# Optimization experiments

Measured on AMD Instinct MI355X. Metric: run time of the kernel, lower is better.

Reference implementation:

```python
import jax, jax.numpy as jnp
import numpy as np

VOC_SIZE = 50000
WORD_DIM = 64
CPR_DIM = 64
NUM_RELS = 7
BATCH = 1024
N_LEAVES = 64  # complete binary tree, depth 6
BOUND = 0.05


def setup_inputs() -> dict:
    key = jax.random.key(0)
    ks = jax.random.split(key, 16)
    u = lambda k, shape: jax.random.uniform(k, shape, jnp.float32, -BOUND, BOUND)
    return {
        "left_leaves": jax.random.randint(ks[0], (BATCH, N_LEAVES), 0, VOC_SIZE),
        "right_leaves": jax.random.randint(ks[1], (BATCH, N_LEAVES), 0, VOC_SIZE),
        "voc_w": u(ks[2], (WORD_DIM, VOC_SIZE)),
        "voc_b": u(ks[3], (WORD_DIM,)),
        "cps_w": u(ks[4], (WORD_DIM, 2 * WORD_DIM)),
        "cps_b": u(ks[5], (WORD_DIM,)),
        "cpst_w": u(ks[6], (WORD_DIM, WORD_DIM * WORD_DIM)),
        "cpst_b": u(ks[7], (WORD_DIM,)),
        "cpr_w": u(ks[8], (CPR_DIM, 2 * WORD_DIM)),
        "cpr_b": u(ks[9], (CPR_DIM,)),
        "cprt_w": u(ks[10], (CPR_DIM, WORD_DIM * WORD_DIM)),
        "cprt_b": u(ks[11], (CPR_DIM,)),
        "sm_w": u(ks[12], (NUM_RELS, CPR_DIM)),
        "sm_b": u(ks[13], (NUM_RELS,)),
    }


def _compose(x, cps_w, cps_b, cpst_w, cpst_b):
    # x: [B, N, d] leaf embeddings of a complete binary tree; reduce level by level.
    B, N, d = x.shape
    while N > 1:
        L = x[:, 0::2, :]  # [B, N/2, d]
        R = x[:, 1::2, :]
        cps = jnp.einsum("bnf,ef->bne", jnp.concatenate([L, R], axis=-1), cps_w) + cps_b
        # NOTE: source computes ger(left, left) for interior nodes (left with itself)
        kron = (L[:, :, :, None] * L[:, :, None, :]).reshape(B, N // 2, d * d)
        cps_t = jnp.einsum("bnk,ek->bne", kron, cpst_w) + cpst_b
        x = jnp.tanh(cps + cps_t)
        N //= 2
    return x[:, 0, :]  # [B, d]


def reference(left_leaves, right_leaves, voc_w, voc_b, cps_w, cps_b, cpst_w, cpst_b,
              cpr_w, cpr_b, cprt_w, cprt_b, sm_w, sm_b):
    # onehot @ Linear == embedding gather of columns of voc_w, plus bias
    left_emb = voc_w.T[left_leaves] + voc_b    # [B, N, d]
    right_emb = voc_w.T[right_leaves] + voc_b
    l = _compose(left_emb, cps_w, cps_b, cpst_w, cpst_b)   # [B, d]
    r = _compose(right_emb, cps_w, cps_b, cpst_w, cpst_b)  # [B, d]
    cpr = jnp.concatenate([l, r], axis=-1) @ cpr_w.T + cpr_b
    kron = (l[:, :, None] * r[:, None, :]).reshape(l.shape[0], -1)  # [B, d*d]
    cpr_t = kron @ cprt_w.T + cprt_b
    act = jax.nn.leaky_relu(cpr + cpr_t, negative_slope=0.01)
    logits = act @ sm_w.T + sm_b
    return jax.nn.softmax(logits, axis=-1)  # [B, num_rels]
```

## Files before the change

### kernel.cpp

```cpp
#include <hip/hip_runtime.h>
#include <hip/hip_bf16.h>
#include <cstdint>
#include <cstddef>

typedef _Float16 f16x8 __attribute__((ext_vector_type(8)));
typedef float    f32x4 __attribute__((ext_vector_type(4)));

#define VOC    50000
#define W2T    2432
#define NSTG_T 19
#define W2F    4224
#define NSTG_F 33
#define STG    8192
#define XSTR   72
#define TPW    8
#define IPW    16

__device__ __attribute__((aligned(256))) unsigned short g_vocT[(size_t)VOC * 64];
__device__ __attribute__((aligned(256))) unsigned short g_roots[2048 * 64];
__device__ __attribute__((aligned(256))) unsigned short g_cpstU[(size_t)NSTG_T * STG];
__device__ __attribute__((aligned(256))) unsigned short g_cprtU[(size_t)NSTG_F * STG];
__device__ float g_smw[7 * 64];
__device__ float g_smb[7];
__device__ float g_biasC[64];
__device__ float g_biasF[64];

#define KE(BI0,BJ0,R0,BI1,BJ1,R1) \
    ((BI0) | ((BJ0) << 3) | ((R0) << 6) | ((BI1) << 7) | ((BJ1) << 10) | ((R1) << 13))
__device__ __constant__ int g_ktab[18] = {
    KE(0,0,1, 0,1,1), KE(0,2,0, 0,3,0), KE(0,4,0, 0,5,0), KE(0,6,0, 0,7,0),
    KE(1,1,1, 1,2,1), KE(1,3,0, 1,4,0), KE(1,5,0, 1,6,0), KE(1,7,0, 2,2,1),
    KE(2,3,1, 2,4,0), KE(2,5,0, 2,6,0), KE(2,7,0, 3,3,1), KE(3,4,1, 3,5,0),
    KE(3,6,0, 3,7,0), KE(4,4,1, 4,5,1), KE(4,6,0, 4,7,0), KE(5,5,1, 5,6,1),
    KE(5,7,0, 6,6,1), KE(6,7,1, 7,7,1)
};

__device__ __forceinline__ float b2f(unsigned short u) {
    unsigned int x = ((unsigned int)u) << 16;
    return __builtin_bit_cast(float, x);
}
__device__ __forceinline__ unsigned short f2b(float f) {
    return __builtin_bit_cast(unsigned short, (__bf16)f);
}
__device__ __forceinline__ unsigned short f2h(float f) {
    return __builtin_bit_cast(unsigned short, (_Float16)f);
}
__device__ __forceinline__ float scrub(float v) {
    return fminf(fmaxf(v, -64.f), 64.f);
}
__device__ __forceinline__ float ldf(const void* p, size_t i, int isb) {
    return isb ? b2f(((const unsigned short*)p)[i]) : ((const float*)p)[i];
}
__device__ __forceinline__ int detect_isb(const void* voc_b) {
    const unsigned int* p = (const unsigned int*)voc_b;
    int ok = 1;
    for (int k = 0; k < 32; k++) {
        float v = b2f((unsigned short)(p[k] & 0xFFFFu));
        if (!(fabsf(v) <= 0.0502f)) ok = 0;
    }
    return ok;
}

__global__ __launch_bounds__(256) void k_prep(
    const void* voc_w, const void* voc_b,
    const void* cps_w, const void* cps_b, const void* cpst_w, const void* cpst_b,
    const void* cpr_w, const void* cpr_b, const void* cprt_w, const void* cprt_b,
    const void* sm_w, const void* sm_b)
{
    __shared__ float tile[64][65];
    __shared__ float vb[64];
    const int isb = detect_isb(voc_b);
    if (blockIdx.x < 512) {
        int gid = blockIdx.x * 256 + threadIdx.x;
        int stride = 512 * 256;
        for (int d = gid; d < 64 * W2T; d += stride) {
            int s    = d / STG;
            int rem  = d - s * STG;
            int kbl  = rem >> 11;
            int rem2 = rem & 2047;
            int nt   = rem2 >> 9;
            int rem3 = rem2 & 511;
            int q    = rem3 >> 7;
            int rem4 = rem3 & 127;
            int sub  = rem4 >> 3;
            int z    = rem4 & 7;
            int n    = nt * 16 + sub;
            int k    = s * 128 + kbl * 32 + q * 8 + z;
            float w;
            if (k < 2304) {
                int b   = k >> 6;
                int p2l = (k >> 5) & 1;
                int bi = 0, remb = b;
                while (remb >= 8 - bi) { remb -= 8 - bi; bi++; }
                int bj = bi + remb;
                int i = bi * 8 + z;
                int j = bj * 8 + 2 * q + p2l;
                w = ldf(cpst_w, (size_t)n * 4096 + i * 64 + j, isb);
                if (bi != bj)
                    w += ldf(cpst_w, (size_t)n * 4096 + j * 64 + i, isb);
            } else {
                w = ldf(cps_w, (size_t)n * 128 + (k - 2304), isb);
            }
            g_cpstU[d] = f2h(w);
        }
        for (int d = gid; d < 64 * W2F; d += stride) {
            int s    = d / STG;
            int rem  = d - s * STG;
            int kbl  = rem >> 11;
            int rem2 = rem & 2047;
            int nt   = rem2 >> 9;
            int rem3 = rem2 & 511;
            int q    = rem3 >> 7;
            int rem4 = rem3 & 127;
            int sub  = rem4 >> 3;
            int z    = rem4 & 7;
            int n    = nt * 16 + sub;
            int k    = s * 128 + kbl * 32 + q * 8 + z;
            float v2 = (k < 4096) ? ldf(cprt_w, (size_t)n * 4096 + k, isb)
                                  : ldf(cpr_w,  (size_t)n * 128 + (k - 4096), isb);
            g_cprtU[d] = f2h(v2);
        }
        for (int i = gid; i < 448; i += stride) g_smw[i] = ldf(sm_w, i, isb);
        if (gid < 64) {
            g_biasC[gid] = ldf(cps_b, gid, isb) + ldf(cpst_b, gid, isb);
            g_biasF[gid] = ldf(cpr_b, gid, isb) + ldf(cprt_b, gid, isb);
        }
        if (gid < 7) g_smb[gid] = ldf(sm_b, gid, isb);
    } else {
        int t = threadIdx.x;
        if (t < 64) vb[t] = ldf(voc_b, t, isb);
        int v0 = (blockIdx.x - 512) * 64;
        int vl = t & 63, dr = t >> 6;
        #pragma unroll
        for (int i = 0; i < 16; i++) {
            int d = dr * 16 + i;
            int v = v0 + vl;
            tile[vl][d] = (v < VOC) ? ldf(voc_w, (size_t)d * VOC + v, isb) : 0.f;
        }
        __syncthreads();
        int dl = t & 63, vr0 = t >> 6;
        #pragma unroll
        for (int i = 0; i < 16; i++) {
            int vr = vr0 * 16 + i;
            int v = v0 + vr;
            if (v < VOC) g_vocT[(size_t)v * 64 + dl] = f2h(tile[vr][dl] + vb[dl]);
        }
    }
}

#define EPILOGUE(CO)                                                          \
    if (lv < 5) {                                                             \
        _Pragma("unroll")                                                     \
        for (int nt = 0; nt < 4; nt++) {                                      \
            int e = nt * 16 + sub;                                            \
            _Pragma("unroll")                                                 \
            for (int rr = 0; rr < 4; rr++) {                                  \
                int m = chv[CO] * 16 + q * 4 + rr;                            \
                if (m < nodes) {                                              \
                    int t2 = m >> lg, n2 = m & (cnew - 1);                    \
                    Xs[(t2 * 64 + n2) * XSTR + e] =                           \
                        f2h(tanhf(scrub(acc[CO][nt][rr] + biasC[e])));        \
                }                                                             \
            }                                                                 \
        }                                                                     \
    } else {                                                                  \
        _Pragma("unroll")                                                     \
        for (int nt = 0; nt < 4; nt++) {                                      \
            int e = nt * 16 + sub;                                            \
            _Pragma("unroll")                                                 \
            for (int rr = 0; rr < 4; rr++) {                                  \
                int m = q * 4 + rr;                                           \
                if (m < TPW)                                                  \
                    g_roots[((size_t)wg * TPW + m) * 64 + e] =                \
                        f2h(tanhf(scrub(acc[CO][nt][rr] + biasC[e])));        \
            }                                                                 \
        }                                                                     \
    }

#define EXSEND(CS)                                                            \
    { _Pragma("unroll")                                                       \
      for (int nt = 0; nt < 4; nt++)                                          \
          *(f32x4*)(exchS + wave * 1024 + nt * 256 + lane * 4) = acc[CS][nt]; }

#define EXRECV(CO)                                                            \
    { _Pragma("unroll")                                                       \
      for (int nt = 0; nt < 4; nt++) {                                        \
          f32x4 v_ = *(const f32x4*)(exchS + (wave ^ 1) * 1024 + nt * 256 + lane * 4); \
          _Pragma("unroll")                                                   \
          for (int z = 0; z < 4; z++) acc[CO][nt][z] += v_[z];                \
      } }

#define BLD8(BF, SBASE)                                                       \
    { const unsigned short* gs_ = (SBASE) + half * 4096 + lane * 8;           \
      _Pragma("unroll")                                                       \
      for (int j = 0; j < 8; j++)                                             \
          BF[j] = *(const f16x8*)(gs_ + (j >> 2) * 2048 + (j & 3) * 512); }

#define KMM(CI, AV, B0, B1, B2, B3)                                           \
    { f16x8 a_ = (AV);                                                        \
      acc[CI][0] = __builtin_amdgcn_mfma_f32_16x16x32_f16(a_, B0, acc[CI][0], 0, 0, 0); \
      acc[CI][1] = __builtin_amdgcn_mfma_f32_16x16x32_f16(a_, B1, acc[CI][1], 0, 0, 0); \
      acc[CI][2] = __builtin_amdgcn_mfma_f32_16x16x32_f16(a_, B2, acc[CI][2], 0, 0, 0); \
      acc[CI][3] = __builtin_amdgcn_mfma_f32_16x16x32_f16(a_, B3, acc[CI][3], 0, 0, 0); }

#define KBLOCKR(BF, BI, BJ, RLD)                                              \
    if (act[0]) {                                                             \
        if (RLD) {                                                            \
            lA0 = *(const f16x8*)(Xs + slotL[0] + (BI) * 8);                  \
            if (act[1]) lA1 = *(const f16x8*)(Xs + slotL[1] + (BI) * 8);      \
            if (act[2]) lA2 = *(const f16x8*)(Xs + slotL[2] + (BI) * 8);      \
            if (act[3]) lA3 = *(const f16x8*)(Xs + slotL[3] + (BI) * 8);      \
        }                                                                     \
        _Float16 sc0[4], sc1[4];                                              \
        _Pragma("unroll")                                                     \
        for (int c = 0; c < 4; c++)                                           \
            if (act[c]) {                                                     \
                unsigned pr_ = *(const unsigned*)(Xs + slotL[c] + (BJ) * 8 + 2 * q); \
                sc0[c] = __builtin_bit_cast(_Float16, (unsigned short)(pr_ & 0xFFFFu)); \
                sc1[c] = __builtin_bit_cast(_Float16, (unsigned short)(pr_ >> 16));     \
            }                                                                 \
        _Pragma("unroll")                                                     \
        for (int p2 = 0; p2 < 2; p2++) {                                      \
            KMM(0, lA0 * (p2 ? sc1[0] : sc0[0]),                              \
                BF[p2 * 4 + 0], BF[p2 * 4 + 1], BF[p2 * 4 + 2], BF[p2 * 4 + 3]) \
            if (act[1]) KMM(1, lA1 * (p2 ? sc1[1] : sc0[1]),                  \
                BF[p2 * 4 + 0], BF[p2 * 4 + 1], BF[p2 * 4 + 2], BF[p2 * 4 + 3]) \
            if (act[2]) KMM(2, lA2 * (p2 ? sc1[2] : sc0[2]),                  \
                BF[p2 * 4 + 0], BF[p2 * 4 + 1], BF[p2 * 4 + 2], BF[p2 * 4 + 3]) \
            if (act[3]) KMM(3, lA3 * (p2 ? sc1[3] : sc0[3]),                  \
                BF[p2 * 4 + 0], BF[p2 * 4 + 1], BF[p2 * 4 + 2], BF[p2 * 4 + 3]) \
        }                                                                     \
    }

#define KRUNR(S, BF)                                                          \
    {                                                                         \
        int e_   = g_ktab[S];                                                 \
        int ent_ = half ? (e_ >> 7) : e_;                                     \
        int bi_  = ent_ & 7;                                                  \
        int bj_  = (ent_ >> 3) & 7;                                           \
        int rld_ = (ent_ >> 6) & 1;                                           \
        KBLOCKR((BF), bi_, bj_, rld_)                                         \
    }

__global__ __launch_bounds__(512, 2)
void k_tree(const int* __restrict__ lleaf, const int* __restrict__ rleaf)
{
    __shared__ __attribute__((aligned(16))) unsigned short Xs[512 * XSTR];
    __shared__ __attribute__((aligned(16))) float exchS[8192];
    __shared__ float biasC[64];
    const int tid = threadIdx.x;
    const int wg  = blockIdx.x;

    if (tid < 64) biasC[tid] = g_biasC[tid];

    {
        int t = tid >> 6, i = tid & 63;
        int gidx = wg * TPW + t;
        int b = (gidx < 1024) ? gidx : gidx - 1024;
        const int* lv2 = (gidx < 1024) ? lleaf : rleaf;
        int idx = lv2[b * 64 + i];
        idx = (idx < 0) ? 0 : ((idx >= VOC) ? VOC - 1 : idx);
        const uint4* src = (const uint4*)(g_vocT + (size_t)idx * 64);
        uint4* dst = (uint4*)(Xs + tid * XSTR);
        #pragma unroll
        for (int z = 0; z < 8; z++) dst[z] = src[z];
    }

    __syncthreads();

    const int lane = tid & 63, wave = tid >> 6;
    const int q = lane >> 4, sub = lane & 15;
    const int p = wave >> 1, half = wave & 1;

    #pragma unroll 1
    for (int lv = 0; lv < 6; lv++) {
        const int lg = 5 - lv;
        const int cnew = 1 << lg;
        const int nodes = TPW << lg;
        const int nchunks = (nodes + 15) >> 4;

        int act[4], chv[4], slotL[4];
        #pragma unroll
        for (int c = 0; c < 4; c++) {
            int ch = p + 4 * c;
            act[c] = (ch < nchunks);
            chv[c] = ch;
            int m = ch * 16 + sub;
            if (!act[c] || m >= nodes) m = 0;
            int t = m >> lg, n = m & (cnew - 1);
            slotL[c] = (t * 64 + 2 * n) * XSTR;
        }

        f16x8 lA0 = {}, lA1 = {}, lA2 = {}, lA3 = {};
        f32x4 acc[4][4];
        #pragma unroll
        for (int c = 0; c < 4; c++)
            #pragma unroll
            for (int nt = 0; nt < 4; nt++)
                #pragma unroll
                for (int z = 0; z < 4; z++) acc[c][nt][z] = 0.f;

        f16x8 bfA[8], bfB[8];
        if (act[0]) BLD8(bfA, g_cpstU)
        #pragma unroll 1
        for (int t = 0; t < 9; t++) {
            if (act[0]) BLD8(bfB, g_cpstU + (size_t)(2 * t + 1) * STG)
            KRUNR(2 * t, bfA)
            if (act[0]) BLD8(bfA, g_cpstU + (size_t)(2 * t + 2) * STG)
            KRUNR(2 * t + 1, bfB)
        }

        if (act[0]) {
            #pragma unroll
            for (int p2 = 0; p2 < 2; p2++) {
                #pragma unroll
                for (int c = 0; c < 4; c++) {
                    if (!act[c]) continue;
                    f16x8 A = *(const f16x8*)(Xs + slotL[c] + half * XSTR + p2 * 32 + q * 8);
                    acc[c][0] = __builtin_amdgcn_mfma_f32_16x16x32_f16(A, bfA[p2 * 4 + 0], acc[c][0], 0, 0, 0);
                    acc[c][1] = __builtin_amdgcn_mfma_f32_16x16x32_f16(A, bfA[p2 * 4 + 1], acc[c][1], 0, 0, 0);
                    acc[c][2] = __builtin_amdgcn_mfma_f32_16x16x32_f16(A, bfA[p2 * 4 + 2], acc[c][2], 0, 0, 0);
                    acc[c][3] = __builtin_amdgcn_mfma_f32_16x16x32_f16(A, bfA[p2 * 4 + 3], acc[c][3], 0, 0, 0);
                }
            }
        }

        if (half == 0) { if (act[1]) EXSEND(1) } else { if (act[0]) EXSEND(0) }
        __syncthreads();
        if (half == 0) {
            if (act[0]) { EXRECV(0) EPILOGUE(0) }
        } else {
            if (act[1]) { EXRECV(1) EPILOGUE(1) }
        }
        __syncthreads();
        if (half == 0) { if (act[3]) EXSEND(3) } else { if (act[2]) EXSEND(2) }
        __syncthreads();
        if (half == 0) {
            if (act[2]) { EXRECV(2) EPILOGUE(2) }
        } else {
            if (act[3]) { EXRECV(3) EPILOGUE(3) }
        }
        __syncthreads();
    }
}

#define BLD4(BF, S)                                                           \
    { const unsigned short* gs_ = g_cprtU + (size_t)(S) * STG + w * 512 + lane * 8; \
      _Pragma("unroll")                                                       \
      for (int j = 0; j < 4; j++)                                             \
          BF[j] = *(const f16x8*)(gs_ + j * 2048); }

#define FKRONR(S, BF)                                                         \
    { _Pragma("unroll")                                                       \
      for (int ii = 0; ii < 2; ii++) {                                        \
          int i_ = 2 * (S) + ii;                                              \
          _Float16 li_ = __builtin_bit_cast(_Float16, Lv[rowLo + i_]);        \
          _Pragma("unroll")                                                   \
          for (int p2 = 0; p2 < 2; p2++) {                                    \
              f16x8 afr_ = Ra[p2] * li_;                                      \
              acc = __builtin_amdgcn_mfma_f32_16x16x32_f16(afr_, BF[2 * ii + p2], acc, 0, 0, 0); \
          }                                                                   \
      } }

__global__ __launch_bounds__(256, 2) void k_final(const void* __restrict__ voc_b,
                                                  void* __restrict__ out)
{
    __shared__ __attribute__((aligned(16))) unsigned short Lv[IPW * XSTR], Rv[IPW * XSTR];
    __shared__ float actS[IPW][65];
    __shared__ float smw[7][64];
    __shared__ float smbS[7];
    __shared__ float biasF[64];
    const int tid = threadIdx.x, wg = blockIdx.x;
    const int isb = detect_isb(voc_b);

    if (tid < 64) biasF[tid] = g_biasF[tid];
    if (tid < 7)  smbS[tid] = g_smb[tid];
    for (int z = tid; z < 448; z += 256) smw[z >> 6][z & 63] = g_smw[z];

    {
        int side = tid >> 7, idx = tid & 127;
        int item = idx >> 3, piece = idx & 7;
        const uint4* s4 = (const uint4*)(g_roots +
            ((size_t)(side * 1024) + (size_t)wg * IPW + item) * 64 + piece * 8);
        uint4* d4 = (uint4*)((side ? Rv : Lv) + item * XSTR + piece * 8);
        *d4 = *s4;
    }

    const int lane = tid & 63, w = tid >> 6;
    const int q = lane >> 4, sub = lane & 15;
    const int rowLo = sub * XSTR;

    f16x8 bA[4], bB[4];
    BLD4(bA, 0)

    __syncthreads();

    f16x8 Ra[2];
    Ra[0] = *(const f16x8*)(Rv + rowLo + q * 8);
    Ra[1] = *(const f16x8*)(Rv + rowLo + 32 + q * 8);

    f32x4 acc;
    #pragma unroll
    for (int z = 0; z < 4; z++) acc[z] = 0.f;

    #pragma unroll 1
    for (int t = 0; t < 16; t++) {
        BLD4(bB, 2 * t + 1)
        FKRONR(2 * t, bA)
        BLD4(bA, 2 * t + 2)
        FKRONR(2 * t + 1, bB)
    }

    {
        f16x8 A4[4];
        A4[0] = *(const f16x8*)(Lv + rowLo + q * 8);
        A4[1] = *(const f16x8*)(Lv + rowLo + 32 + q * 8);
        A4[2] = *(const f16x8*)(Rv + rowLo + q * 8);
        A4[3] = *(const f16x8*)(Rv + rowLo + 32 + q * 8);
        #pragma unroll
        for (int kbl = 0; kbl < 4; kbl++)
            acc = __builtin_amdgcn_mfma_f32_16x16x32_f16(A4[kbl], bA[kbl], acc, 0, 0, 0);
    }

    {
        int e = w * 16 + sub;
        #pragma unroll
        for (int rr = 0; rr < 4; rr++) {
            int item = q * 4 + rr;
            float v = scrub(acc[rr] + biasF[e]);
            v = (v > 0.f) ? v : 0.01f * v;
            actS[item][e] = v;
        }
    }
    __syncthreads();

    if (tid < IPW) {
        float lg[7];
        #pragma unroll
        for (int j = 0; j < 7; j++) lg[j] = smbS[j];
        for (int e = 0; e < 64; e++) {
            float a = actS[tid][e];
            #pragma unroll
            for (int j = 0; j < 7; j++) lg[j] += smw[j][e] * a;
        }
        float mx = lg[0];
        #pragma unroll
        for (int j = 1; j < 7; j++) mx = fmaxf(mx, lg[j]);
        float s = 0.f, pr[7];
        #pragma unroll
        for (int j = 0; j < 7; j++) { pr[j] = expf(lg[j] - mx); s += pr[j]; }
        float inv = 1.f / s;
        size_t b = (size_t)wg * IPW + tid;
        if (isb) {
            unsigned short* o = (unsigned short*)out;
            #pragma unroll
            for (int j = 0; j < 7; j++) o[b * 7 + j] = f2b(pr[j] * inv);
        } else {
            float* o = (float*)out;
            #pragma unroll
            for (int j = 0; j < 7; j++) o[b * 7 + j] = pr[j] * inv;
        }
    }
}

extern "C" void kernel_launch(void* const* d_in, const int* in_sizes, int n_in,
                              void* d_out, int out_size, void* d_ws, size_t ws_size,
                              hipStream_t stream) {
    const int* lleaf = (const int*)d_in[0];
    const int* rleaf = (const int*)d_in[1];
    const void* voc_w  = d_in[2];
    const void* voc_b  = d_in[3];
    const void* cps_w  = d_in[4];
    const void* cps_b  = d_in[5];
    const void* cpst_w = d_in[6];
    const void* cpst_b = d_in[7];
    const void* cpr_w  = d_in[8];
    const void* cpr_b  = d_in[9];
    const void* cprt_w = d_in[10];
    const void* cprt_b = d_in[11];
    const void* sm_w   = d_in[12];
    const void* sm_b   = d_in[13];

    k_prep<<<512 + (VOC + 63) / 64, 256, 0, stream>>>(
        voc_w, voc_b, cps_w, cps_b, cpst_w, cpst_b,
        cpr_w, cpr_b, cprt_w, cprt_b, sm_w, sm_b);
    k_tree<<<2048 / TPW, 512, 0, stream>>>(lleaf, rleaf);
    k_final<<<64, 256, 0, stream>>>(voc_b, (unsigned short*)d_out);
}
```

Baseline: 177.3 us.

## Fuse prep, tree and final kernels into one cooperative persistent kernel

Merges the three launches (weight/vocab prep, tree composition, final classifier) into one cooperative kernel of 256 blocks of 512 threads, using grid-wide syncs between phases. Shared memory is reused across phases, for example the transpose tile is aliased onto Xs. This removes the launch gaps between kernels and the tail idle time of each one. In exchange, the vocabulary transpose now runs on fewer blocks, occupancy is limited by cooperative-launch residency rules, and each grid sync has its own cost.

```diff
diff --git a/kernel.cpp b/kernel.cpp
--- a/kernel.cpp
+++ b/kernel.cpp
@@ -1,7 +1,10 @@
 #include <hip/hip_runtime.h>
 #include <hip/hip_bf16.h>
+#include <hip/hip_cooperative_groups.h>
 #include <cstdint>
 #include <cstddef>
+
+namespace cg = cooperative_groups;
 
 typedef _Float16 f16x8 __attribute__((ext_vector_type(8)));
 typedef float    f32x4 __attribute__((ext_vector_type(4)));
@@ -61,18 +64,136 @@
     return ok;
 }
 
-__global__ __launch_bounds__(256) void k_prep(
-    const void* voc_w, const void* voc_b,
-    const void* cps_w, const void* cps_b, const void* cpst_w, const void* cpst_b,
-    const void* cpr_w, const void* cpr_b, const void* cprt_w, const void* cprt_b,
-    const void* sm_w, const void* sm_b)
+#define EPILOGUE(CO)                                                          \
+    if (lv < 5) {                                                             \
+        _Pragma("unroll")                                                     \
+        for (int nt = 0; nt < 4; nt++) {                                      \
+            int e = nt * 16 + sub;                                            \
+            _Pragma("unroll")                                                 \
+            for (int rr = 0; rr < 4; rr++) {                                  \
+                int m = chv[CO] * 16 + q * 4 + rr;                            \
+                if (m < nodes) {                                              \
+                    int t2 = m >> lg, n2 = m & (cnew - 1);                    \
+                    Xs[(t2 * 64 + n2) * XSTR + e] =                           \
+                        f2h(tanhf(scrub(acc[CO][nt][rr] + biasC[e])));        \
+                }                                                             \
+            }                                                                 \
+        }                                                                     \
+    } else {                                                                  \
+        _Pragma("unroll")                                                     \
+        for (int nt = 0; nt < 4; nt++) {                                      \
+            int e = nt * 16 + sub;                                            \
+            _Pragma("unroll")                                                 \
+            for (int rr = 0; rr < 4; rr++) {                                  \
+                int m = q * 4 + rr;                                           \
+                if (m < TPW)                                                  \
+                    g_roots[((size_t)wg * TPW + m) * 64 + e] =                \
+                        f2h(tanhf(scrub(acc[CO][nt][rr] + biasC[e])));        \
+            }                                                                 \
+        }                                                                     \
+    }
+
+#define EXSEND(CS)                                                            \
+    { _Pragma("unroll")                                                       \
+      for (int nt = 0; nt < 4; nt++)                                          \
+          *(f32x4*)(exchS + wave * 1024 + nt * 256 + lane * 4) = acc[CS][nt]; }
+
+#define EXRECV(CO)                                                            \
+    { _Pragma("unroll")                                                       \
+      for (int nt = 0; nt < 4; nt++) {                                        \
+          f32x4 v_ = *(const f32x4*)(exchS + (wave ^ 1) * 1024 + nt * 256 + lane * 4); \
+          _Pragma("unroll")                                                   \
+          for (int z = 0; z < 4; z++) acc[CO][nt][z] += v_[z];                \
+      } }
+
+#define BLD8(BF, SBASE)                                                       \
+    { const unsigned short* gs_ = (SBASE) + half * 4096 + lane * 8;           \
+      _Pragma("unroll")                                                       \
+      for (int j = 0; j < 8; j++)                                             \
+          BF[j] = *(const f16x8*)(gs_ + (j >> 2) * 2048 + (j & 3) * 512); }
+
+#define KMM(CI, AV, B0, B1, B2, B3)                                           \
+    { f16x8 a_ = (AV);                                                        \
+      acc[CI][0] = __builtin_amdgcn_mfma_f32_16x16x32_f16(a_, B0, acc[CI][0], 0, 0, 0); \
+      acc[CI][1] = __builtin_amdgcn_mfma_f32_16x16x32_f16(a_, B1, acc[CI][1], 0, 0, 0); \
+      acc[CI][2] = __builtin_amdgcn_mfma_f32_16x16x32_f16(a_, B2, acc[CI][2], 0, 0, 0); \
+      acc[CI][3] = __builtin_amdgcn_mfma_f32_16x16x32_f16(a_, B3, acc[CI][3], 0, 0, 0); }
+
+#define KBLOCKR(BF, BI, BJ, RLD)                                              \
+    if (act[0]) {                                                             \
+        if (RLD) {                                                            \
+            lA0 = *(const f16x8*)(Xs + slotL[0] + (BI) * 8);                  \
+            if (act[1]) lA1 = *(const f16x8*)(Xs + slotL[1] + (BI) * 8);      \
+            if (act[2]) lA2 = *(const f16x8*)(Xs + slotL[2] + (BI) * 8);      \
+            if (act[3]) lA3 = *(const f16x8*)(Xs + slotL[3] + (BI) * 8);      \
+        }                                                                     \
+        _Float16 sc0[4], sc1[4];                                              \
+        _Pragma("unroll")                                                     \
+        for (int c = 0; c < 4; c++)                                           \
+            if (act[c]) {                                                     \
+                unsigned pr_ = *(const unsigned*)(Xs + slotL[c] + (BJ) * 8 + 2 * q); \
+                sc0[c] = __builtin_bit_cast(_Float16, (unsigned short)(pr_ & 0xFFFFu)); \
+                sc1[c] = __builtin_bit_cast(_Float16, (unsigned short)(pr_ >> 16));     \
+            }                                                                 \
+        _Pragma("unroll")                                                     \
+        for (int p2 = 0; p2 < 2; p2++) {                                      \
+            KMM(0, lA0 * (p2 ? sc1[0] : sc0[0]),                              \
+                BF[p2 * 4 + 0], BF[p2 * 4 + 1], BF[p2 * 4 + 2], BF[p2 * 4 + 3]) \
+            if (act[1]) KMM(1, lA1 * (p2 ? sc1[1] : sc0[1]),                  \
+                BF[p2 * 4 + 0], BF[p2 * 4 + 1], BF[p2 * 4 + 2], BF[p2 * 4 + 3]) \
+            if (act[2]) KMM(2, lA2 * (p2 ? sc1[2] : sc0[2]),                  \
+                BF[p2 * 4 + 0], BF[p2 * 4 + 1], BF[p2 * 4 + 2], BF[p2 * 4 + 3]) \
+            if (act[3]) KMM(3, lA3 * (p2 ? sc1[3] : sc0[3]),                  \
+                BF[p2 * 4 + 0], BF[p2 * 4 + 1], BF[p2 * 4 + 2], BF[p2 * 4 + 3]) \
+        }                                                                     \
+    }
+
+#define KRUNR(S, BF)                                                          \
+    {                                                                         \
+        int e_   = g_ktab[S];                                                 \
+        int ent_ = half ? (e_ >> 7) : e_;                                     \
+        int bi_  = ent_ & 7;                                                  \
+        int bj_  = (ent_ >> 3) & 7;                                           \
+        int rld_ = (ent_ >> 6) & 1;                                           \
+        KBLOCKR((BF), bi_, bj_, rld_)                                         \
+    }
+
+#define BLD4(BF, S)                                                           \
+    { const unsigned short* gs_ = g_cprtU + (size_t)(S) * STG + w * 512 + lane * 8; \
+      _Pragma("unroll")                                                       \
+      for (int j = 0; j < 4; j++)                                             \
+          BF[j] = *(const f16x8*)(gs_ + j * 2048); }
+
+#define FKRONR(S, BF)                                                         \
+    { _Pragma("unroll")                                                       \
+      for (int ii = 0; ii < 2; ii++) {                                        \
+          int i_ = 2 * (S) + ii;                                              \
+          _Float16 li_ = __builtin_bit_cast(_Float16, Lv[rowLo + i_]);        \
+          _Pragma("unroll")                                                   \
+          for (int p2 = 0; p2 < 2; p2++) {                                    \
+              f16x8 afr_ = Ra[p2] * li_;                                      \
+              accF = __builtin_amdgcn_mfma_f32_16x16x32_f16(afr_, BF[2 * ii + p2], accF, 0, 0, 0); \
+          }                                                                   \
+      } }
+
+__global__ __launch_bounds__(512, 2)
+void k_all(const int* __restrict__ lleaf, const int* __restrict__ rleaf,
+           const void* __restrict__ voc_w, const void* __restrict__ voc_b,
+           const void* cps_w, const void* cps_b, const void* cpst_w, const void* cpst_b,
+           const void* cpr_w, const void* cpr_b, const void* cprt_w, const void* cprt_b,
+           const void* sm_w, const void* sm_b, void* __restrict__ out)
 {
-    __shared__ float tile[64][65];
-    __shared__ float vb[64];
+    __shared__ __attribute__((aligned(16))) unsigned short Xs[512 * XSTR];
+    __shared__ __attribute__((aligned(16))) float exchS[8192];
+    __shared__ float biasC[64];
+    const int tid = threadIdx.x;
+    const int wg  = blockIdx.x;
     const int isb = detect_isb(voc_b);
-    if (blockIdx.x < 512) {
-        int gid = blockIdx.x * 256 + threadIdx.x;
-        int stride = 512 * 256;
+    cg::grid_group grid = cg::this_grid();
+
+    {
+        int gid = wg * 512 + tid;
+        const int stride = 256 * 512;
         for (int d = gid; d < 64 * W2T; d += stride) {
             int s    = d / STG;
             int rem  = d - s * STG;
@@ -126,133 +247,35 @@
             g_biasF[gid] = ldf(cpr_b, gid, isb) + ldf(cprt_b, gid, isb);
         }
         if (gid < 7) g_smb[gid] = ldf(sm_b, gid, isb);
-    } else {
-        int t = threadIdx.x;
-        if (t < 64) vb[t] = ldf(voc_b, t, isb);
-        int v0 = (blockIdx.x - 512) * 64;
-        int vl = t & 63, dr = t >> 6;
-        #pragma unroll
-        for (int i = 0; i < 16; i++) {
-            int d = dr * 16 + i;
-            int v = v0 + vl;
-            tile[vl][d] = (v < VOC) ? ldf(voc_w, (size_t)d * VOC + v, isb) : 0.f;
-        }
+
+        float* tileF = (float*)Xs;
+        float* vbF   = exchS;
+        if (tid < 64) vbF[tid] = ldf(voc_b, tid, isb);
         __syncthreads();
-        int dl = t & 63, vr0 = t >> 6;
-        #pragma unroll
-        for (int i = 0; i < 16; i++) {
-            int vr = vr0 * 16 + i;
-            int v = v0 + vr;
-            if (v < VOC) g_vocT[(size_t)v * 64 + dl] = f2h(tile[vr][dl] + vb[dl]);
-        }
-    }
-}
-
-#define EPILOGUE(CO)                                                          \
-    if (lv < 5) {                                                             \
-        _Pragma("unroll")                                                     \
-        for (int nt = 0; nt < 4; nt++) {                                      \
-            int e = nt * 16 + sub;                                            \
-            _Pragma("unroll")                                                 \
-            for (int rr = 0; rr < 4; rr++) {                                  \
-                int m = chv[CO] * 16 + q * 4 + rr;                            \
-                if (m < nodes) {                                              \
-                    int t2 = m >> lg, n2 = m & (cnew - 1);                    \
-                    Xs[(t2 * 64 + n2) * XSTR + e] =                           \
-                        f2h(tanhf(scrub(acc[CO][nt][rr] + biasC[e])));        \
-                }                                                             \
-            }                                                                 \
-        }                                                                     \
-    } else {                                                                  \
-        _Pragma("unroll")                                                     \
-        for (int nt = 0; nt < 4; nt++) {                                      \
-            int e = nt * 16 + sub;                                            \
-            _Pragma("unroll")                                                 \
-            for (int rr = 0; rr < 4; rr++) {                                  \
-                int m = q * 4 + rr;                                           \
-                if (m < TPW)                                                  \
-                    g_roots[((size_t)wg * TPW + m) * 64 + e] =                \
-                        f2h(tanhf(scrub(acc[CO][nt][rr] + biasC[e])));        \
-            }                                                                 \
-        }                                                                     \
-    }
-
-#define EXSEND(CS)                                                            \
-    { _Pragma("unroll")                                                       \
-      for (int nt = 0; nt < 4; nt++)                                          \
-          *(f32x4*)(exchS + wave * 1024 + nt * 256 + lane * 4) = acc[CS][nt]; }
-
-#define EXRECV(CO)                                                            \
-    { _Pragma("unroll")                                                       \
-      for (int nt = 0; nt < 4; nt++) {                                        \
-          f32x4 v_ = *(const f32x4*)(exchS + (wave ^ 1) * 1024 + nt * 256 + lane * 4); \
-          _Pragma("unroll")                                                   \
-          for (int z = 0; z < 4; z++) acc[CO][nt][z] += v_[z];                \
-      } }
-
-#define BLD8(BF, SBASE)                                                       \
-    { const unsigned short* gs_ = (SBASE) + half * 4096 + lane * 8;           \
-      _Pragma("unroll")                                                       \
-      for (int j = 0; j < 8; j++)                                             \
-          BF[j] = *(const f16x8*)(gs_ + (j >> 2) * 2048 + (j & 3) * 512); }
-
-#define KMM(CI, AV, B0, B1, B2, B3)                                           \
-    { f16x8 a_ = (AV);                                                        \
-      acc[CI][0] = __builtin_amdgcn_mfma_f32_16x16x32_f16(a_, B0, acc[CI][0], 0, 0, 0); \
-      acc[CI][1] = __builtin_amdgcn_mfma_f32_16x16x32_f16(a_, B1, acc[CI][1], 0, 0, 0); \
-      acc[CI][2] = __builtin_amdgcn_mfma_f32_16x16x32_f16(a_, B2, acc[CI][2], 0, 0, 0); \
-      acc[CI][3] = __builtin_amdgcn_mfma_f32_16x16x32_f16(a_, B3, acc[CI][3], 0, 0, 0); }
-
-#define KBLOCKR(BF, BI, BJ, RLD)                                              \
-    if (act[0]) {                                                             \
-        if (RLD) {                                                            \
-            lA0 = *(const f16x8*)(Xs + slotL[0] + (BI) * 8);                  \
-            if (act[1]) lA1 = *(const f16x8*)(Xs + slotL[1] + (BI) * 8);      \
-            if (act[2]) lA2 = *(const f16x8*)(Xs + slotL[2] + (BI) * 8);      \
-            if (act[3]) lA3 = *(const f16x8*)(Xs + slotL[3] + (BI) * 8);      \
-        }                                                                     \
-        _Float16 sc0[4], sc1[4];                                              \
-        _Pragma("unroll")                                                     \
-        for (int c = 0; c < 4; c++)                                           \
-            if (act[c]) {                                                     \
-                unsigned pr_ = *(const unsigned*)(Xs + slotL[c] + (BJ) * 8 + 2 * q); \
-                sc0[c] = __builtin_bit_cast(_Float16, (unsigned short)(pr_ & 0xFFFFu)); \
-                sc1[c] = __builtin_bit_cast(_Float16, (unsigned short)(pr_ >> 16));     \
-            }                                                                 \
-        _Pragma("unroll")                                                     \
-        for (int p2 = 0; p2 < 2; p2++) {                                      \
-            KMM(0, lA0 * (p2 ? sc1[0] : sc0[0]),                              \
-                BF[p2 * 4 + 0], BF[p2 * 4 + 1], BF[p2 * 4 + 2], BF[p2 * 4 + 3]) \
-            if (act[1]) KMM(1, lA1 * (p2 ? sc1[1] : sc0[1]),                  \
-                BF[p2 * 4 + 0], BF[p2 * 4 + 1], BF[p2 * 4 + 2], BF[p2 * 4 + 3]) \
-            if (act[2]) KMM(2, lA2 * (p2 ? sc1[2] : sc0[2]),                  \
-                BF[p2 * 4 + 0], BF[p2 * 4 + 1], BF[p2 * 4 + 2], BF[p2 * 4 + 3]) \
-            if (act[3]) KMM(3, lA3 * (p2 ? sc1[3] : sc0[3]),                  \
-                BF[p2 * 4 + 0], BF[p2 * 4 + 1], BF[p2 * 4 + 2], BF[p2 * 4 + 3]) \
-        }                                                                     \
-    }
-
-#define KRUNR(S, BF)                                                          \
-    {                                                                         \
-        int e_   = g_ktab[S];                                                 \
-        int ent_ = half ? (e_ >> 7) : e_;                                     \
-        int bi_  = ent_ & 7;                                                  \
-        int bj_  = (ent_ >> 3) & 7;                                           \
-        int rld_ = (ent_ >> 6) & 1;                                           \
-        KBLOCKR((BF), bi_, bj_, rld_)                                         \
-    }
-
-__global__ __launch_bounds__(512, 2)
-void k_tree(const int* __restrict__ lleaf, const int* __restrict__ rleaf)
-{
-    __shared__ __attribute__((aligned(16))) unsigned short Xs[512 * XSTR];
-    __shared__ __attribute__((aligned(16))) float exchS[8192];
-    __shared__ float biasC[64];
-    const int tid = threadIdx.x;
-    const int wg  = blockIdx.x;
+        for (int vt = wg; vt < (VOC + 63) / 64; vt += 256) {
+            int v0 = vt * 64;
+            int vl = tid & 63, dr = tid >> 6;
+            #pragma unroll
+            for (int i = 0; i < 8; i++) {
+                int d = dr * 8 + i;
+                int v = v0 + vl;
+                tileF[vl * 65 + d] = (v < VOC) ? ldf(voc_w, (size_t)d * VOC + v, isb) : 0.f;
+            }
+            __syncthreads();
+            int dl = tid & 63, vr0 = tid >> 6;
+            #pragma unroll
+            for (int i = 0; i < 8; i++) {
+                int vr = vr0 * 8 + i;
+                int v = v0 + vr;
+                if (v < VOC) g_vocT[(size_t)v * 64 + dl] = f2h(tileF[vr * 65 + dl] + vbF[dl]);
+            }
+            __syncthreads();
+        }
+    }
+    __threadfence();
+    grid.sync();
 
     if (tid < 64) biasC[tid] = g_biasC[tid];
-
     {
         int t = tid >> 6, i = tid & 63;
         int gidx = wg * TPW + t;
@@ -265,200 +288,173 @@
         #pragma unroll
         for (int z = 0; z < 8; z++) dst[z] = src[z];
     }
-
     __syncthreads();
 
-    const int lane = tid & 63, wave = tid >> 6;
-    const int q = lane >> 4, sub = lane & 15;
-    const int p = wave >> 1, half = wave & 1;
-
-    #pragma unroll 1
-    for (int lv = 0; lv < 6; lv++) {
-        const int lg = 5 - lv;
-        const int cnew = 1 << lg;
-        const int nodes = TPW << lg;
-        const int nchunks = (nodes + 15) >> 4;
-
-        int act[4], chv[4], slotL[4];
-        #pragma unroll
-        for (int c = 0; c < 4; c++) {
-            int ch = p + 4 * c;
-            act[c] = (ch < nchunks);
-            chv[c] = ch;
-            int m = ch * 16 + sub;
-            if (!act[c] || m >= nodes) m = 0;
-            int t = m >> lg, n = m & (cnew - 1);
-            slotL[c] = (t * 64 + 2 * n) * XSTR;
-        }
-
-        f16x8 lA0 = {}, lA1 = {}, lA2 = {}, lA3 = {};
-        f32x4 acc[4][4];
-        #pragma unroll
-        for (int c = 0; c < 4; c++)
-            #pragma unroll
-            for (int nt = 0; nt < 4; nt++)
-                #pragma unroll
-                for (int z = 0; z < 4; z++) acc[c][nt][z] = 0.f;
-
-        f16x8 bfA[8], bfB[8];
-        if (act[0]) BLD8(bfA, g_cpstU)
+    {
+        const int lane = tid & 63, wave = tid >> 6;
+        const int q = lane >> 4, sub = lane & 15;
+        const int p = wave >> 1, half = wave & 1;
+
         #pragma unroll 1
-        for (int t = 0; t < 9; t++) {
-            if (act[0]) BLD8(bfB, g_cpstU + (size_t)(2 * t + 1) * STG)
-            KRUNR(2 * t, bfA)
-            if (act[0]) BLD8(bfA, g_cpstU + (size_t)(2 * t + 2) * STG)
-            KRUNR(2 * t + 1, bfB)
-        }
-
-        if (act[0]) {
-            #pragma unroll
-            for (int p2 = 0; p2 < 2; p2++) {
-                #pragma unroll
-                for (int c = 0; c < 4; c++) {
-                    if (!act[c]) continue;
-                    f16x8 A = *(const f16x8*)(Xs + slotL[c] + half * XSTR + p2 * 32 + q * 8);
-                    acc[c][0] = __builtin_amdgcn_mfma_f32_16x16x32_f16(A, bfA[p2 * 4 + 0], acc[c][0], 0, 0, 0);
-                    acc[c][1] = __builtin_amdgcn_mfma_f32_16x16x32_f16(A, bfA[p2 * 4 + 1], acc[c][1], 0, 0, 0);
-                    acc[c][2] = __builtin_amdgcn_mfma_f32_16x16x32_f16(A, bfA[p2 * 4 + 2], acc[c][2], 0, 0, 0);
-                    acc[c][3] = __builtin_amdgcn_mfma_f32_16x16x32_f16(A, bfA[p2 * 4 + 3], acc[c][3], 0, 0, 0);
+        for (int lv = 0; lv < 6; lv++) {
+            const int lg = 5 - lv;
+            const int cnew = 1 << lg;
+            const int nodes = TPW << lg;
+            const int nchunks = (nodes + 15) >> 4;
+
+            int act[4], chv[4], slotL[4];
+            #pragma unroll
+            for (int c = 0; c < 4; c++) {
+                int ch = p + 4 * c;
+                act[c] = (ch < nchunks);
+                chv[c] = ch;
+                int m = ch * 16 + sub;
+                if (!act[c] || m >= nodes) m = 0;
+                int t = m >> lg, n = m & (cnew - 1);
+                slotL[c] = (t * 64 + 2 * n) * XSTR;
+            }
+
+            f16x8 lA0 = {}, lA1 = {}, lA2 = {}, lA3 = {};
+            f32x4 acc[4][4];
+            #pragma unroll
+            for (int c = 0; c < 4; c++)
+                #pragma unroll
+                for (int nt = 0; nt < 4; nt++)
+                    #pragma unroll
+                    for (int z = 0; z < 4; z++) acc[c][nt][z] = 0.f;
+
+            f16x8 bfA[8], bfB[8];
+            if (act[0]) BLD8(bfA, g_cpstU)
+            #pragma unroll 1
+            for (int t = 0; t < 9; t++) {
+                if (act[0]) BLD8(bfB, g_cpstU + (size_t)(2 * t + 1) * STG)
+                KRUNR(2 * t, bfA)
+                if (act[0]) BLD8(bfA, g_cpstU + (size_t)(2 * t + 2) * STG)
+                KRUNR(2 * t + 1, bfB)
+            }
+            if (act[0]) {
+                #pragma unroll
+                for (int p2 = 0; p2 < 2; p2++) {
+                    #pragma unroll
+                    for (int c = 0; c < 4; c++) {
+                        if (!act[c]) continue;
+                        f16x8 A = *(const f16x8*)(Xs + slotL[c] + half * XSTR + p2 * 32 + q * 8);
+                        acc[c][0] = __builtin_amdgcn_mfma_f32_16x16x32_f16(A, bfA[p2 * 4 + 0], acc[c][0], 0, 0, 0);
+                        acc[c][1] = __builtin_amdgcn_mfma_f32_16x16x32_f16(A, bfA[p2 * 4 + 1], acc[c][1], 0, 0, 0);
+                        acc[c][2] = __builtin_amdgcn_mfma_f32_16x16x32_f16(A, bfA[p2 * 4 + 2], acc[c][2], 0, 0, 0);
+                        acc[c][3] = __builtin_amdgcn_mfma_f32_16x16x32_f16(A, bfA[p2 * 4 + 3], acc[c][3], 0, 0, 0);
+                    }
                 }
             }
-        }
-
-        if (half == 0) { if (act[1]) EXSEND(1) } else { if (act[0]) EXSEND(0) }
+
+            if (half == 0) { if (act[1]) EXSEND(1) } else { if (act[0]) EXSEND(0) }
+            __syncthreads();
+            if (half == 0) {
+                if (act[0]) { EXRECV(0) EPILOGUE(0) }
+            } else {
+                if (act[1]) { EXRECV(1) EPILOGUE(1) }
+            }
+            __syncthreads();
+            if (half == 0) { if (act[3]) EXSEND(3) } else { if (act[2]) EXSEND(2) }
+            __syncthreads();
+            if (half == 0) {
+                if (act[2]) { EXRECV(2) EPILOGUE(2) }
+            } else {
+                if (act[3]) { EXRECV(3) EPILOGUE(3) }
+            }
+            __syncthreads();
+        }
+    }
+    __threadfence();
+    grid.sync();
+
+    if (wg < 64) {
+        unsigned short* Lv = Xs;
+        unsigned short* Rv = Xs + IPW * XSTR;
+        float* actS  = exchS;
+        float* smwS  = exchS + 1040;
+        float* smbS  = exchS + 1488;
+        float* biasF = exchS + 1496;
+
+        if (tid < 64) biasF[tid] = g_biasF[tid];
+        if (tid < 7)  smbS[tid] = g_smb[tid];
+        for (int z = tid; z < 448; z += 512) smwS[z] = g_smw[z];
+        if (tid < 256) {
+            int side = tid >> 7, idx = tid & 127;
+            int item = idx >> 3, piece = idx & 7;
+            const uint4* s4 = (const uint4*)(g_roots +
+                ((size_t)(side * 1024) + (size_t)wg * IPW + item) * 64 + piece * 8);
+            uint4* d4 = (uint4*)((side ? Rv : Lv) + item * XSTR + piece * 8);
+            *d4 = *s4;
+        }
         __syncthreads();
-        if (half == 0) {
-            if (act[0]) { EXRECV(0) EPILOGUE(0) }
-        } else {
-            if (act[1]) { EXRECV(1) EPILOGUE(1) }
+
+        if (tid < 256) {
+            const int lane = tid & 63, w = tid >> 6;
+            const int q = lane >> 4, sub = lane & 15;
+            const int rowLo = sub * XSTR;
+
+            f16x8 bA[4], bB[4];
+            BLD4(bA, 0)
+            f16x8 Ra[2];
+            Ra[0] = *(const f16x8*)(Rv + rowLo + q * 8);
+            Ra[1] = *(const f16x8*)(Rv + rowLo + 32 + q * 8);
+            f32x4 accF = {0.f, 0.f, 0.f, 0.f};
+
+            #pragma unroll 1
+            for (int t = 0; t < 16; t++) {
+                BLD4(bB, 2 * t + 1)
+                FKRONR(2 * t, bA)
+                BLD4(bA, 2 * t + 2)
+                FKRONR(2 * t + 1, bB)
+            }
+            {
+                f16x8 A4[4];
+                A4[0] = *(const f16x8*)(Lv + rowLo + q * 8);
+                A4[1] = *(const f16x8*)(Lv + rowLo + 32 + q * 8);
+                A4[2] = *(const f16x8*)(Rv + rowLo + q * 8);
+                A4[3] = *(const f16x8*)(Rv + rowLo + 32 + q * 8);
+                #pragma unroll
+                for (int kbl = 0; kbl < 4; kbl++)
+                    accF = __builtin_amdgcn_mfma_f32_16x16x32_f16(A4[kbl], bA[kbl], accF, 0, 0, 0);
+            }
+            int e = w * 16 + sub;
+            #pragma unroll
+            for (int rr = 0; rr < 4; rr++) {
+                int item = q * 4 + rr;
+                float v = scrub(accF[rr] + biasF[e]);
+                v = (v > 0.f) ? v : 0.01f * v;
+                actS[item * 65 + e] = v;
+            }
         }
         __syncthreads();
-        if (half == 0) { if (act[3]) EXSEND(3) } else { if (act[2]) EXSEND(2) }
-        __syncthreads();
-        if (half == 0) {
-            if (act[2]) { EXRECV(2) EPILOGUE(2) }
-        } else {
-            if (act[3]) { EXRECV(3) EPILOGUE(3) }
-        }
-        __syncthreads();
-    }
-}
-
-#define BLD4(BF, S)                                                           \
-    { const unsigned short* gs_ = g_cprtU + (size_t)(S) * STG + w * 512 + lane * 8; \
-      _Pragma("unroll")                                                       \
-      for (int j = 0; j < 4; j++)                                             \
-          BF[j] = *(const f16x8*)(gs_ + j * 2048); }
-
-#define FKRONR(S, BF)                                                         \
-    { _Pragma("unroll")                                                       \
-      for (int ii = 0; ii < 2; ii++) {                                        \
-          int i_ = 2 * (S) + ii;                                              \
-          _Float16 li_ = __builtin_bit_cast(_Float16, Lv[rowLo + i_]);        \
-          _Pragma("unroll")                                                   \
-          for (int p2 = 0; p2 < 2; p2++) {                                    \
-              f16x8 afr_ = Ra[p2] * li_;                                      \
-              acc = __builtin_amdgcn_mfma_f32_16x16x32_f16(afr_, BF[2 * ii + p2], acc, 0, 0, 0); \
-          }                                                                   \
-      } }
-
-__global__ __launch_bounds__(256, 2) void k_final(const void* __restrict__ voc_b,
-                                                  void* __restrict__ out)
-{
-    __shared__ __attribute__((aligned(16))) unsigned short Lv[IPW * XSTR], Rv[IPW * XSTR];
-    __shared__ float actS[IPW][65];
-    __shared__ float smw[7][64];
-    __shared__ float smbS[7];
-    __shared__ float biasF[64];
-    const int tid = threadIdx.x, wg = blockIdx.x;
-    const int isb = detect_isb(voc_b);
-
-    if (tid < 64) biasF[tid] = g_biasF[tid];
-    if (tid < 7)  smbS[tid] = g_smb[tid];
-    for (int z = tid; z < 448; z += 256) smw[z >> 6][z & 63] = g_smw[z];
-
-    {
-        int side = tid >> 7, idx = tid & 127;
-        int item = idx >> 3, piece = idx & 7;
-        const uint4* s4 = (const uint4*)(g_roots +
-            ((size_t)(side * 1024) + (size_t)wg * IPW + item) * 64 + piece * 8);
-        uint4* d4 = (uint4*)((side ? Rv : Lv) + item * XSTR + piece * 8);
-        *d4 = *s4;
-    }
-
-    const int lane = tid & 63, w = tid >> 6;
-    const int q = lane >> 4, sub = lane & 15;
-    const int rowLo = sub * XSTR;
-
-    f16x8 bA[4], bB[4];
-    BLD4(bA, 0)
-
-    __syncthreads();
-
-    f16x8 Ra[2];
-    Ra[0] = *(const f16x8*)(Rv + rowLo + q * 8);
-    Ra[1] = *(const f16x8*)(Rv + rowLo + 32 + q * 8);
-
-    f32x4 acc;
-    #pragma unroll
-    for (int z = 0; z < 4; z++) acc[z] = 0.f;
-
-    #pragma unroll 1
-    for (int t = 0; t < 16; t++) {
-        BLD4(bB, 2 * t + 1)
-        FKRONR(2 * t, bA)
-        BLD4(bA, 2 * t + 2)
-        FKRONR(2 * t + 1, bB)
-    }
-
-    {
-        f16x8 A4[4];
-        A4[0] = *(const f16x8*)(Lv + rowLo + q * 8);
-        A4[1] = *(const f16x8*)(Lv + rowLo + 32 + q * 8);
-        A4[2] = *(const f16x8*)(Rv + rowLo + q * 8);
-        A4[3] = *(const f16x8*)(Rv + rowLo + 32 + q * 8);
-        #pragma unroll
-        for (int kbl = 0; kbl < 4; kbl++)
-            acc = __builtin_amdgcn_mfma_f32_16x16x32_f16(A4[kbl], bA[kbl], acc, 0, 0, 0);
-    }
-
-    {
-        int e = w * 16 + sub;
-        #pragma unroll
-        for (int rr = 0; rr < 4; rr++) {
-            int item = q * 4 + rr;
-            float v = scrub(acc[rr] + biasF[e]);
-            v = (v > 0.f) ? v : 0.01f * v;
-            actS[item][e] = v;
-        }
-    }
-    __syncthreads();
-
-    if (tid < IPW) {
-        float lg[7];
-        #pragma unroll
-        for (int j = 0; j < 7; j++) lg[j] = smbS[j];
-        for (int e = 0; e < 64; e++) {
-            float a = actS[tid][e];
-            #pragma unroll
-            for (int j = 0; j < 7; j++) lg[j] += smw[j][e] * a;
-        }
-        float mx = lg[0];
-        #pragma unroll
-        for (int j = 1; j < 7; j++) mx = fmaxf(mx, lg[j]);
-        float s = 0.f, pr[7];
-        #pragma unroll
-        for (int j = 0; j < 7; j++) { pr[j] = expf(lg[j] - mx); s += pr[j]; }
-        float inv = 1.f / s;
-        size_t b = (size_t)wg * IPW + tid;
-        if (isb) {
-            unsigned short* o = (unsigned short*)out;
-            #pragma unroll
-            for (int j = 0; j < 7; j++) o[b * 7 + j] = f2b(pr[j] * inv);
-        } else {
-            float* o = (float*)out;
-            #pragma unroll
-            for (int j = 0; j < 7; j++) o[b * 7 + j] = pr[j] * inv;
+
+        if (tid < IPW) {
+            float lg[7];
+            #pragma unroll
+            for (int j = 0; j < 7; j++) lg[j] = smbS[j];
+            for (int e = 0; e < 64; e++) {
+                float a = actS[tid * 65 + e];
+                #pragma unroll
+                for (int j = 0; j < 7; j++) lg[j] += smwS[j * 64 + e] * a;
+            }
+            float mx = lg[0];
+            #pragma unroll
+            for (int j = 1; j < 7; j++) mx = fmaxf(mx, lg[j]);
+            float s = 0.f, pr[7];
+            #pragma unroll
+            for (int j = 0; j < 7; j++) { pr[j] = expf(lg[j] - mx); s += pr[j]; }
+            float inv = 1.f / s;
+            size_t b = (size_t)wg * IPW + tid;
+            if (isb) {
+                unsigned short* o = (unsigned short*)out;
+                #pragma unroll
+                for (int j = 0; j < 7; j++) o[b * 7 + j] = f2b(pr[j] * inv);
+            } else {
+                float* o = (float*)out;
+                #pragma unroll
+                for (int j = 0; j < 7; j++) o[b * 7 + j] = pr[j] * inv;
+            }
         }
     }
 }
@@ -480,10 +476,13 @@
     const void* cprt_b = d_in[11];
     const void* sm_w   = d_in[12];
     const void* sm_b   = d_in[13];
-
-    k_prep<<<512 + (VOC + 63) / 64, 256, 0, stream>>>(
-        voc_w, voc_b, cps_w, cps_b, cpst_w, cpst_b,
-        cpr_w, cpr_b, cprt_w, cprt_b, sm_w, sm_b);
-    k_tree<<<2048 / TPW, 512, 0, stream>>>(lleaf, rleaf);
-    k_final<<<64, 256, 0, stream>>>(voc_b, (unsigned short*)d_out);
-}
+    void* out = d_out;
+
+    void* args[] = {
+        (void*)&lleaf, (void*)&rleaf, (void*)&voc_w, (void*)&voc_b,
+        (void*)&cps_w, (void*)&cps_b, (void*)&cpst_w, (void*)&cpst_b,
+        (void*)&cpr_w, (void*)&cpr_b, (void*)&cprt_w, (void*)&cprt_b,
+        (void*)&sm_w, (void*)&sm_b, (void*)&out
+    };
+    hipLaunchCooperativeKernel(k_all, dim3(256), dim3(512), args, 0, stream);
+}
```

After: 343.9 us. 94.0% more time.
